# Performance work log

Measured on AMD Instinct MI355X. Metric: run time of the kernel, lower is better.

Reference implementation:

```python
import jax, jax.numpy as jnp
import numpy as np
import math

B, N, DEG, C, F0, NCLS = 128, 512, 8, 128, 128, 10
E = B * N * DEG
RATIO = 0.8
K1 = math.ceil(RATIO * N)    # 410
K2 = math.ceil(RATIO * K1)   # 328
K3 = math.ceil(RATIO * K2)   # 263


def setup_inputs() -> dict:
    key = jax.random.key(0)
    ks = jax.random.split(key, 32)
    x = jax.random.normal(ks[0], (B * N, F0), jnp.float32)
    epg = N * DEG
    src_l = jax.random.randint(ks[1], (B, epg), 0, N)
    dst_l = jax.random.randint(ks[2], (B, epg), 0, N)
    off = (jnp.arange(B, dtype=jnp.int32) * N)[:, None]
    edge_src = (src_l + off).reshape(-1).astype(jnp.int32)
    edge_dst = (dst_l + off).reshape(-1).astype(jnp.int32)

    def lin(k, fi, fo):
        return jax.random.normal(k, (fi, fo), jnp.float32) / np.float32(np.sqrt(fi))

    inp = {"x": x, "edge_src": edge_src, "edge_dst": edge_dst}
    i = 3
    for s, fi in (("1", F0), ("2", C), ("3", C)):
        inp["Wroot" + s] = lin(ks[i], fi, C); i += 1
        inp["Wrel" + s] = lin(ks[i], fi, C); i += 1
        inp["brel" + s] = jnp.zeros((C,), jnp.float32)
        inp["p" + s] = jax.random.normal(ks[i], (C,), jnp.float32); i += 1
    inp["W1"] = lin(ks[i], 2 * C, 128); i += 1
    inp["b1"] = jnp.zeros((128,), jnp.float32)
    inp["W2"] = lin(ks[i], 128, 64); i += 1
    inp["b2"] = jnp.zeros((64,), jnp.float32)
    inp["W3"] = lin(ks[i], 64, NCLS); i += 1
    inp["b3"] = jnp.zeros((NCLS,), jnp.float32)
    return inp


def graph_conv(x, src, dst, emask, Wroot, Wrel, brel, num_nodes):
    # PyG GraphConv (aggr='add'): lin_rel(sum_j x_j) + lin_root(x_i)
    msg = x[src] * emask[:, None]                      # masked gather  [E, C]
    agg = jax.ops.segment_sum(msg, dst, num_segments=num_nodes)
    return agg @ Wrel + brel + x @ Wroot


def topk_pool(x, p, src, dst, emask, b, n, k):
    # score = tanh(x . p / ||p||), keep top-k nodes per graph, scale kept x by score
    score = jnp.tanh((x @ p) / jnp.linalg.norm(p))     # [b*n]
    vals, idx = jax.lax.top_k(score.reshape(b, n), k)  # [b, k]
    perm = (idx + (jnp.arange(b, dtype=idx.dtype) * n)[:, None]).reshape(-1)
    x_new = x[perm] * vals.reshape(-1, 1)
    inv = jnp.full((b * n,), -1, jnp.int32).at[perm].set(
        jnp.arange(b * k, dtype=jnp.int32))
    ns, nd = inv[src], inv[dst]
    nmask = emask * (ns >= 0) * (nd >= 0)
    return x_new, jnp.maximum(ns, 0), jnp.maximum(nd, 0), nmask


def readout(h, b, k):
    hb = h.reshape(b, k, -1)
    return jnp.concatenate([hb.max(axis=1), hb.mean(axis=1)], axis=-1)  # gmp||gap


def reference(x, edge_src, edge_dst,
              Wroot1, Wrel1, brel1, p1,
              Wroot2, Wrel2, brel2, p2,
              Wroot3, Wrel3, brel3, p3,
              W1, b1, W2, b2, W3, b3):
    emask = jnp.ones((E,), x.dtype)
    s, d = edge_src, edge_dst

    h = jax.nn.relu(graph_conv(x, s, d, emask, Wroot1, Wrel1, brel1, B * N))
    h, s, d, emask = topk_pool(h, p1, s, d, emask, B, N, K1)
    x1 = readout(h, B, K1)

    h = jax.nn.relu(graph_conv(h, s, d, emask, Wroot2, Wrel2, brel2, B * K1))
    h, s, d, emask = topk_pool(h, p2, s, d, emask, B, K1, K2)
    x2 = readout(h, B, K2)

    h = jax.nn.relu(graph_conv(h, s, d, emask, Wroot3, Wrel3, brel3, B * K2))
    h, s, d, emask = topk_pool(h, p3, s, d, emask, B, K2, K3)
    x3 = readout(h, B, K3)

    g = x1 + x2 + x3                                   # [B, 256]
    g = jax.nn.relu(g @ W1 + b1)                       # dropout is identity in eval
    g = jax.nn.relu(g @ W2 + b2)
    return jax.nn.log_softmax(g @ W3 + b3, axis=-1)    # [B, NCLS]
```

## Files before the change

kernel.cpp:

```cpp
#include <hip/hip_runtime.h>
#include <hip/hip_bf16.h>
#include <math.h>

#define B_G   128
#define N0    512
#define DEG   8
#define CCH   128
#define EPG   (N0*DEG)
#define E_TOTAL (B_G*EPG)
#define K1    410
#define K2    328
#define K3    263
#define NCLS  10

#define SWZ(row, cb) ((((cb) ^ ((row) & 7)) << 2))

using bf16x8 = __attribute__((ext_vector_type(8))) __bf16;
using f32x4  = __attribute__((ext_vector_type(4))) float;
typedef unsigned short ushort;
typedef unsigned int uint;
typedef unsigned long long u64;

__device__ __forceinline__ ushort f2b(float f) {
    uint u = __float_as_uint(f);
    u += 0x7fffu + ((u >> 16) & 1u);
    return (ushort)(u >> 16);
}
__device__ __forceinline__ float b2f(ushort h) {
    return __uint_as_float(((uint)h) << 16);
}
__device__ __forceinline__ void split2(float v, ushort& hi, ushort& lo) {
    hi = f2b(v);
    lo = f2b(v - b2f(hi));
}
__device__ __forceinline__ uint pksplit(float v) {
    ushort h, l; split2(v, h, l);
    return (uint)h | ((uint)l << 16);
}
__device__ __forceinline__ float unpk(uint u) {
    return __uint_as_float(u << 16) + __uint_as_float(u & 0xffff0000u);
}
__device__ __forceinline__ float keyval(u64 key) {
    uint tu = (uint)(key >> 32);
    uint su = (tu & 0x80000000u) ? (tu & 0x7fffffffu) : ~tu;
    return __uint_as_float(su);
}

__global__ __launch_bounds__(512) void setup_kernel(
        const float* __restrict__ Wrel0, const float* __restrict__ Wroot0,
        const float* __restrict__ Wrel1, const float* __restrict__ Wroot1,
        const float* __restrict__ Wrel2, const float* __restrict__ Wroot2,
        ushort* __restrict__ Bph, ushort* __restrict__ Bpl,
        const int* __restrict__ es, const int* __restrict__ ed,
        int* __restrict__ indptr0, int* __restrict__ counts0, ushort* __restrict__ srclist0) {
    __shared__ uint epk[EPG];
    __shared__ int cnt[512], pref[512], curs[512];
    if (blockIdx.x < B_G) {
        int b = blockIdx.x, tid = threadIdx.x;
        cnt[tid] = 0;
        __syncthreads();
        int base = b * EPG;
        for (int i = tid; i < EPG; i += 512) {
            int s = es[base + i] & (N0 - 1);
            int d = ed[base + i] & (N0 - 1);
            epk[i] = (uint)s | ((uint)d << 16);
            atomicAdd(&cnt[d], 1);
        }
        __syncthreads();
        pref[tid] = cnt[tid];
        __syncthreads();
        for (int off = 1; off < 512; off <<= 1) {
            int v = (tid >= off) ? pref[tid - off] : 0;
            __syncthreads();
            pref[tid] += v;
            __syncthreads();
        }
        int excl = tid ? pref[tid - 1] : 0;
        indptr0[b * N0 + tid] = base + excl;
        counts0[b * N0 + tid] = cnt[tid];
        curs[tid] = excl;
        __syncthreads();
        for (int i = tid; i < EPG; i += 512) {
            uint wv = epk[i];
            int dl = wv >> 16;
            int pos = atomicAdd(&curs[dl], 1);
            srclist0[base + pos] = (ushort)(wv & 0xFFFFu);
        }
    } else {
        int i = (blockIdx.x - B_G) * 512 + threadIdx.x;
        if (i < 3 * 32768) {
            int layer = i >> 15, rem = i & 32767;
            int j = rem & 7, lane = (rem >> 3) & 63, cf = (rem >> 9) & 7, ks = rem >> 12;
            int k = ks * 32 + (lane >> 4) * 8 + j;
            int c = cf * 16 + (lane & 15);
            const float* Wrel  = layer == 0 ? Wrel0  : layer == 1 ? Wrel1  : Wrel2;
            const float* Wroot = layer == 0 ? Wroot0 : layer == 1 ? Wroot1 : Wroot2;
            float v = (k < 128) ? Wrel[k * 128 + c] : Wroot[(k - 128) * 128 + c];
            ushort hi, lo; split2(v, hi, lo);
            Bph[i] = hi; Bpl[i] = lo;
        }
    }
}

__global__ __launch_bounds__(1024) void aggregate0(
        const float* __restrict__ xf,
        const int* __restrict__ indptr, const int* __restrict__ counts,
        const ushort* __restrict__ srclist,
        uint* __restrict__ aggp) {
    extern __shared__ float slab[];
    int b = blockIdx.x >> 2, q = blockIdx.x & 3;
    int tid = threadIdx.x;
    const float4* xf4 = (const float4*)xf;
    for (int t = tid; t < N0 * 8; t += 1024) {
        int nd = t >> 3, c4 = t & 7;
        float4 u = xf4[(size_t)(b * N0 + nd) * 32 + q * 8 + c4];
        *(float4*)&slab[nd * 32 + SWZ(nd, c4)] = u;
    }
    __syncthreads();
    int wave = tid >> 6, lane = tid & 63;
    int gl = lane >> 3, sub = lane & 7;
    for (int g = wave; g < N0 / 8; g += 16) {
        int d = g * 8 + gl;
        int beg = indptr[b * N0 + d];
        int cnt = counts[b * N0 + d];
        float4 acc = make_float4(0.f, 0.f, 0.f, 0.f);
        int id_next = (cnt > 0) ? (int)srclist[beg] : 0;
        for (int j = 0; j < cnt; j++) {
            int id = id_next;
            if (j + 1 < cnt) id_next = (int)srclist[beg + j + 1];
            const float4 v = *(const float4*)&slab[id * 32 + SWZ(id, sub)];
            acc.x += v.x; acc.y += v.y; acc.z += v.z; acc.w += v.w;
        }
        uint4 o;
        o.x = pksplit(acc.x); o.y = pksplit(acc.y);
        o.z = pksplit(acc.z); o.w = pksplit(acc.w);
        *(uint4*)&aggp[(size_t)(b * N0 + d) * CCH + q * 32 + sub * 4] = o;
    }
}

__global__ __launch_bounds__(512, 4) void transform_mfma(
        const uint* __restrict__ aggp, const uint* __restrict__ rootp,
        const float* __restrict__ rootf,
        const ushort* __restrict__ Bph, const ushort* __restrict__ Bpl,
        const float* __restrict__ brel, const float* __restrict__ pvec,
        uint* __restrict__ hout, float* __restrict__ score) {
    __shared__ ushort ldsBh[16384];
    __shared__ ushort ldsBl[16384];
    int tid = threadIdx.x;
    int wave = tid >> 6, lane = tid & 63;
    int r = lane & 15, kb = lane >> 4;
    int rows0 = blockIdx.x * 128 + wave * 16;
    int gid = rows0 + r;

    f32x4 acc[8];
#pragma unroll
    for (int cf = 0; cf < 8; cf++) acc[cf] = (f32x4)(0.f);

    union U16 { uint u[4]; bf16x8 v; };

#pragma unroll
    for (int half = 0; half < 2; half++) {
        if (half) __syncthreads();
#pragma unroll
        for (int i = 0; i < 4; i++) {
            int idx = tid + i * 512;
            ((uint4*)ldsBh)[idx] = ((const uint4*)(Bph + half * 16384))[idx];
            ((uint4*)ldsBl)[idx] = ((const uint4*)(Bpl + half * 16384))[idx];
        }
        __syncthreads();
#pragma unroll
        for (int ks4 = 0; ks4 < 4; ks4++) {
            U16 ah, al;
            if (half && rootf) {
                const float* R = rootf + (size_t)gid * CCH + ks4 * 32 + kb * 8;
                float4 f0 = *(const float4*)R;
                float4 f1 = *(const float4*)(R + 4);
                float c[8] = {f0.x, f0.y, f0.z, f0.w, f1.x, f1.y, f1.z, f1.w};
#pragma unroll
                for (int p2 = 0; p2 < 4; p2++) {
                    ushort h0, l0, h1, l1;
                    split2(c[2 * p2], h0, l0);
                    split2(c[2 * p2 + 1], h1, l1);
                    ah.u[p2] = (uint)h0 | ((uint)h1 << 16);
                    al.u[p2] = (uint)l0 | ((uint)l1 << 16);
                }
            } else {
                const uint* A = half ? rootp : aggp;
                size_t rowbase = (size_t)gid * CCH + ks4 * 32 + kb * 8;
                uint4 ua = *(const uint4*)&A[rowbase];
                uint4 ub = *(const uint4*)&A[rowbase + 4];
                ah.u[0] = (ua.x & 0xffffu) | (ua.y << 16);
                ah.u[1] = (ua.z & 0xffffu) | (ua.w << 16);
                ah.u[2] = (ub.x & 0xffffu) | (ub.y << 16);
                ah.u[3] = (ub.z & 0xffffu) | (ub.w << 16);
                al.u[0] = (ua.x >> 16) | (ua.y & 0xffff0000u);
                al.u[1] = (ua.z >> 16) | (ua.w & 0xffff0000u);
                al.u[2] = (ub.x >> 16) | (ub.y & 0xffff0000u);
                al.u[3] = (ub.z >> 16) | (ub.w & 0xffff0000u);
            }
#pragma unroll
            for (int cf = 0; cf < 8; cf++) {
                bf16x8 bh = *(const bf16x8*)&ldsBh[((ks4 * 8 + cf) * 64 + lane) * 8];
                bf16x8 bl = *(const bf16x8*)&ldsBl[((ks4 * 8 + cf) * 64 + lane) * 8];
                acc[cf] = __builtin_amdgcn_mfma_f32_16x16x32_bf16(ah.v, bl, acc[cf], 0, 0, 0);
                acc[cf] = __builtin_amdgcn_mfma_f32_16x16x32_bf16(al.v, bh, acc[cf], 0, 0, 0);
                acc[cf] = __builtin_amdgcn_mfma_f32_16x16x32_bf16(ah.v, bh, acc[cf], 0, 0, 0);
            }
        }
    }

    float pv[8], bb[8], q = 0.f;
#pragma unroll
    for (int cf = 0; cf < 8; cf++) {
        pv[cf] = pvec[cf * 16 + r];
        bb[cf] = brel[cf * 16 + r];
        q += pv[cf] * pv[cf];
    }
    float dots[4] = {0.f, 0.f, 0.f, 0.f};
#pragma unroll
    for (int cf = 0; cf < 8; cf++) {
#pragma unroll
        for (int reg = 0; reg < 4; reg++) {
            float v = acc[cf][reg] + bb[cf];
            v = v > 0.f ? v : 0.f;
            hout[(size_t)(rows0 + kb * 4 + reg) * CCH + cf * 16 + r] = pksplit(v);
            dots[reg] += v * pv[cf];
        }
    }
#pragma unroll
    for (int off = 1; off < 16; off <<= 1) {
        q += __shfl_xor(q, off);
#pragma unroll
        for (int reg = 0; reg < 4; reg++) dots[reg] += __shfl_xor(dots[reg], off);
    }
    if (r == 0) {
        float inv_norm = rsqrtf(q);
#pragma unroll
        for (int reg = 0; reg < 4; reg++)
            score[rows0 + kb * 4 + reg] = tanhf(dots[reg] * inv_norm);
    }
}

__global__ __launch_bounds__(1024) void pool_kernel(
        const float* __restrict__ score, const uint* __restrict__ hp,
        float* __restrict__ gpart,
        const int* __restrict__ ipt_in, const int* __restrict__ cnt_in,
        const ushort* __restrict__ src_in,
        int* __restrict__ ipt_out, int* __restrict__ cnt_out,
        ushort* __restrict__ src_out,
        uint* __restrict__ pooledX, uint* __restrict__ aggout,
        int n, int k, int do_next) {
    int b = blockIdx.x >> 2, q = blockIdx.x & 3;
    int tid = threadIdx.x;
    __shared__ u64 keys[512];
    __shared__ short invl[512];
    __shared__ float redbuf[1024];
    __shared__ int prefL[512];
    __shared__ int wtot[8], woff[8];
    extern __shared__ float slab[];

    u64 key = 0ull;
    if (tid < 512) {
        if (tid < n) {
            uint u = __float_as_uint(score[b * n + tid]);
            u = (u & 0x80000000u) ? ~u : (u | 0x80000000u);
            key = ((u64)u << 32) | (uint)(~tid);
        }
        invl[tid] = -1;
        for (int kk2 = 2; kk2 <= 64; kk2 <<= 1) {
            for (int j = kk2 >> 1; j > 0; j >>= 1) {
                u64 p = __shfl_xor(key, j);
                bool desc = ((tid & kk2) == 0);
                bool lower = ((tid & j) == 0);
                u64 mx = key > p ? key : p;
                u64 mn = key > p ? p : key;
                key = (desc == lower) ? mx : mn;
            }
        }
    } else {
        for (int t = tid - 512; t < n * 8; t += 512) {
            int nd = t >> 3, c4 = t & 7;
            uint4 u = *(const uint4*)&hp[(size_t)(b * n + nd) * CCH + q * 32 + c4 * 4];
            *(float4*)&slab[nd * 32 + SWZ(nd, c4)] =
                make_float4(unpk(u.x), unpk(u.y), unpk(u.z), unpk(u.w));
        }
    }
    __syncthreads();
    for (int kk2 = 128; kk2 <= 512; kk2 <<= 1) {
        for (int j = kk2 >> 1; j > 0; j >>= 1) {
            if (j >= 64) {
                if (tid < 512) keys[tid] = key;
                __syncthreads();
                if (tid < 512) {
                    u64 p = keys[tid ^ j];
                    bool desc = ((tid & kk2) == 0);
                    bool lower = ((tid & j) == 0);
                    u64 mx = key > p ? key : p;
                    u64 mn = key > p ? p : key;
                    key = (desc == lower) ? mx : mn;
                }
                __syncthreads();
            } else if (tid < 512) {
                u64 p = __shfl_xor(key, j);
                bool desc = ((tid & kk2) == 0);
                bool lower = ((tid & j) == 0);
                u64 mx = key > p ? key : p;
                u64 mn = key > p ? p : key;
                key = (desc == lower) ? mx : mn;
            }
        }
    }
    if (tid < 512) keys[tid] = key;
    __syncthreads();
    if (tid < k) invl[(int)(~(uint)key)] = (short)tid;
    __syncthreads();
    for (int t = tid; t < k * 8; t += 1024) {
        int rank = t >> 3, c4 = t & 7;
        u64 kk = keys[rank];
        int old = (int)(~(uint)kk);
        float v = keyval(kk);
        float* p = &slab[old * 32 + SWZ(old, c4)];
        p[0] *= v; p[1] *= v; p[2] *= v; p[3] *= v;
    }
    __syncthreads();
    if (tid < 512) {
        int w = tid >> 5, ch = tid & 31;
        float mx = -1e30f, sm = 0.f;
        for (int r2 = w; r2 < k; r2 += 16) {
            int old = (int)(~(uint)keys[r2]);
            float v = slab[old * 32 + SWZ(old, ch >> 2) + (ch & 3)];
            mx = fmaxf(mx, v); sm += v;
        }
        redbuf[w * 32 + ch] = mx;
        redbuf[512 + w * 32 + ch] = sm;
    }
    __syncthreads();
    if (tid < 32) {
        float m = -1e30f, s = 0.f;
        for (int w = 0; w < 16; w++) {
            m = fmaxf(m, redbuf[w * 32 + tid]);
            s += redbuf[512 + w * 32 + tid];
        }
        gpart[b * 256 + q * 32 + tid] = m;
        gpart[b * 256 + 128 + q * 32 + tid] = s / (float)k;
    }
    if (!do_next) return;
    for (int t = tid; t < k * 8; t += 1024) {
        int rank = t >> 3, c4 = t & 7;
        int old = (int)(~(uint)keys[rank]);
        const float* p = &slab[old * 32 + SWZ(old, c4)];
        uint4 o;
        o.x = pksplit(p[0]); o.y = pksplit(p[1]);
        o.z = pksplit(p[2]); o.w = pksplit(p[3]);
        *(uint4*)&pooledX[(size_t)(b * k + rank) * CCH + q * 32 + c4 * 4] = o;
    }
    {
        int wave = tid >> 6, lane = tid & 63;
        int gl = lane >> 3, sub = lane & 7;
        int ngroups = (k + 7) >> 3;
        for (int g = wave; g < ngroups; g += 16) {
            int d = g * 8 + gl;
            bool act = d < k;
            int beg = 0, cc = 0;
            if (act) {
                int old = (int)(~(uint)keys[d]);
                beg = ipt_in[b * n + old];
                cc = cnt_in[b * n + old];
            }
            float4 acc = make_float4(0.f, 0.f, 0.f, 0.f);
            int s_next = (cc > 0) ? (int)src_in[beg] : 0;
            for (int j = 0; j < cc; j++) {
                int s = s_next;
                if (j + 1 < cc) s_next = (int)src_in[beg + j + 1];
                if (invl[s] >= 0) {
                    const float4 v = *(const float4*)&slab[s * 32 + SWZ(s, sub)];
                    acc.x += v.x; acc.y += v.y; acc.z += v.z; acc.w += v.w;
                }
            }
            if (act) {
                uint4 o;
                o.x = pksplit(acc.x); o.y = pksplit(acc.y);
                o.z = pksplit(acc.z); o.w = pksplit(acc.w);
                *(uint4*)&aggout[(size_t)(b * k + d) * CCH + q * 32 + sub * 4] = o;
            }
        }
    }
    if (q == 0) {
        int beg = 0, c = 0, nk = 0;
        if (tid < k) {
            int old = (int)(~(uint)keys[tid]);
            beg = ipt_in[b * n + old];
            c = cnt_in[b * n + old];
            for (int t = 0; t < c; t++)
                if (invl[src_in[beg + t]] >= 0) nk++;
        }
        int lane = tid & 63;
        int incl = (tid < 512 && tid < k) ? nk : 0;
#pragma unroll
        for (int o = 1; o < 64; o <<= 1) {
            int t = __shfl_up(incl, o);
            if (lane >= o) incl += t;
        }
        if (tid < 512 && lane == 63) wtot[tid >> 6] = incl;
        __syncthreads();
        if (tid < 8) {
            int s = 0;
            for (int w = 0; w < tid; w++) s += wtot[w];
            woff[tid] = s;
        }
        __syncthreads();
        if (tid < 512) prefL[tid] = incl + woff[tid >> 6];
        __syncthreads();
        if (tid < k) {
            int excl = tid ? prefL[tid - 1] : 0;
            ipt_out[b * k + tid] = b * EPG + excl;
            cnt_out[b * k + tid] = nk;
            int pos = b * EPG + excl;
            for (int t = 0; t < c; t++) {
                int ns = invl[src_in[beg + t]];
                if (ns >= 0) src_out[pos++] = (ushort)ns;
            }
        }
    }
}

__global__ __launch_bounds__(128) void mlp_kernel(const float* __restrict__ gpart,
        const float* __restrict__ W1, const float* __restrict__ b1,
        const float* __restrict__ W2, const float* __restrict__ b2,
        const float* __restrict__ W3, const float* __restrict__ b3,
        float* __restrict__ out) {
    int b = blockIdx.x, t = threadIdx.x;
    __shared__ float gs[256], h1[128], h2[64], lg[10];
    const float* g0 = gpart + ((size_t)0 * B_G + b) * 256;
    const float* g1 = gpart + ((size_t)1 * B_G + b) * 256;
    const float* g2 = gpart + ((size_t)2 * B_G + b) * 256;
    gs[t] = g0[t] + g1[t] + g2[t];
    gs[128 + t] = g0[128 + t] + g1[128 + t] + g2[128 + t];
    __syncthreads();
    {
        float a = b1[t];
        for (int c = 0; c < 256; c++) a += gs[c] * W1[c * 128 + t];
        h1[t] = fmaxf(a, 0.f);
    }
    __syncthreads();
    if (t < 64) {
        float a = b2[t];
        for (int c = 0; c < 128; c++) a += h1[c] * W2[c * 64 + t];
        h2[t] = fmaxf(a, 0.f);
    }
    __syncthreads();
    if (t < 10) {
        float a = b3[t];
        for (int c = 0; c < 64; c++) a += h2[c] * W3[c * 10 + t];
        lg[t] = a;
    }
    __syncthreads();
    if (t < 10) {
        float m = lg[0];
        for (int i = 1; i < 10; i++) m = fmaxf(m, lg[i]);
        float s = 0.f;
        for (int i = 0; i < 10; i++) s += expf(lg[i] - m);
        out[b * 10 + t] = lg[t] - m - logf(s);
    }
}

extern "C" void kernel_launch(void* const* d_in, const int* in_sizes, int n_in,
                              void* d_out, int out_size, void* d_ws, size_t ws_size,
                              hipStream_t stream) {
    (void)in_sizes; (void)n_in; (void)out_size; (void)ws_size;
    const float* x0 = (const float*)d_in[0];
    const int* es = (const int*)d_in[1];
    const int* ed = (const int*)d_in[2];
    const float* Wroot[3] = {(const float*)d_in[3], (const float*)d_in[7], (const float*)d_in[11]};
    const float* Wrel[3]  = {(const float*)d_in[4], (const float*)d_in[8], (const float*)d_in[12]};
    const float* brel[3]  = {(const float*)d_in[5], (const float*)d_in[9], (const float*)d_in[13]};
    const float* pvec[3]  = {(const float*)d_in[6], (const float*)d_in[10], (const float*)d_in[14]};
    const float* W1 = (const float*)d_in[15];
    const float* b1 = (const float*)d_in[16];
    const float* W2 = (const float*)d_in[17];
    const float* b2 = (const float*)d_in[18];
    const float* W3 = (const float*)d_in[19];
    const float* b3 = (const float*)d_in[20];

    size_t off = 0;
    char* base = (char*)d_ws;
    auto alloc = [&](size_t bytes) -> void* {
        void* p = base + off;
        off += (bytes + 255) & ~(size_t)255;
        return p;
    };
    const size_t FEATP = (size_t)(B_G * N0) * CCH * 4;
    uint* P0 = (uint*)alloc(FEATP);
    uint* P1 = (uint*)alloc(FEATP);
    uint* P2 = (uint*)alloc(FEATP);
    ushort* Bph = (ushort*)alloc((size_t)3 * 32768 * 2);
    ushort* Bpl = (ushort*)alloc((size_t)3 * 32768 * 2);
    int* iptA = (int*)alloc((size_t)(B_G * N0) * 4);
    int* cntA = (int*)alloc((size_t)(B_G * N0) * 4);
    ushort* srcA = (ushort*)alloc((size_t)E_TOTAL * 2);
    int* iptB = (int*)alloc((size_t)(B_G * N0) * 4);
    int* cntB = (int*)alloc((size_t)(B_G * N0) * 4);
    ushort* srcB = (ushort*)alloc((size_t)E_TOTAL * 2);
    float* score = (float*)alloc((size_t)(B_G * N0) * 4);
    float* gpart = (float*)alloc((size_t)3 * B_G * 256 * 4);

    setup_kernel<<<B_G + (3 * 32768 + 511) / 512, 512, 0, stream>>>(
        Wrel[0], Wroot[0], Wrel[1], Wroot[1], Wrel[2], Wroot[2],
        Bph, Bpl, es, ed, iptA, cntA, srcA);

    aggregate0<<<4 * B_G, 1024, (size_t)N0 * 32 * 4, stream>>>(
        x0, iptA, cntA, srcA, P1);
    transform_mfma<<<B_G * N0 / 128, 512, 0, stream>>>(
        P1, nullptr, x0, Bph, Bpl, brel[0], pvec[0], P0, score);
    pool_kernel<<<4 * B_G, 1024, (size_t)N0 * 32 * 4, stream>>>(
        score, P0, gpart + (size_t)0 * B_G * 256,
        iptA, cntA, srcA, iptB, cntB, srcB, P2, P1, N0, K1, 1);

    transform_mfma<<<B_G * K1 / 128, 512, 0, stream>>>(
        P1, P2, nullptr, Bph + 32768, Bpl + 32768, brel[1], pvec[1], P0, score);
    pool_kernel<<<4 * B_G, 1024, (size_t)K1 * 32 * 4, stream>>>(
        score, P0, gpart + (size_t)1 * B_G * 256,
        iptB, cntB, srcB, iptA, cntA, srcA, P2, P1, K1, K2, 1);

    transform_mfma<<<B_G * K2 / 128, 512, 0, stream>>>(
        P1, P2, nullptr, Bph + 2 * 32768, Bpl + 2 * 32768, brel[2], pvec[2], P0, score);
    pool_kernel<<<4 * B_G, 1024, (size_t)K2 * 32 * 4, stream>>>(
        score, P0, gpart + (size_t)2 * B_G * 256,
        iptA, cntA, srcA, nullptr, nullptr, nullptr, nullptr, nullptr, K2, K3, 0);

    mlp_kernel<<<B_G, 128, 0, stream>>>(gpart, W1, b1, W2, b2, W3, b3, (float*)d_out);
}
```

Measured before the change: 197.8 us.

## Fuse final top-k pooling and readout into the MLP head kernel

Replaces the last pool_kernel launch (4 blocks per graph, 1024 threads) and the separate MLP kernel with one pool_final kernel per graph. It does a 512-thread bitonic sort of the scores, reads the kept rows directly from global memory to compute the max and mean readout, and then runs the MLP and log-softmax. This removes one launch and the gpart round trip, and skips the slab staging in the final stage, at the cost of fewer, larger blocks (128 instead of 512) doing the final gather. The do_next flag is dropped because the remaining pool_kernel calls always continue.

```diff
diff --git a/kernel.cpp b/kernel.cpp
--- a/kernel.cpp
+++ b/kernel.cpp
@@ -249,7 +249,7 @@
         int* __restrict__ ipt_out, int* __restrict__ cnt_out,
         ushort* __restrict__ src_out,
         uint* __restrict__ pooledX, uint* __restrict__ aggout,
-        int n, int k, int do_next) {
+        int n, int k) {
     int b = blockIdx.x >> 2, q = blockIdx.x & 3;
     int tid = threadIdx.x;
     __shared__ u64 keys[512];
@@ -344,7 +344,6 @@
         gpart[b * 256 + q * 32 + tid] = m;
         gpart[b * 256 + 128 + q * 32 + tid] = s / (float)k;
     }
-    if (!do_next) return;
     for (int t = tid; t < k * 8; t += 1024) {
         int rank = t >> 3, c4 = t & 7;
         int old = (int)(~(uint)keys[rank]);
@@ -424,43 +423,97 @@
     }
 }
 
-__global__ __launch_bounds__(128) void mlp_kernel(const float* __restrict__ gpart,
+__global__ __launch_bounds__(512) void pool_final(
+        const float* __restrict__ score, const uint* __restrict__ hp,
+        const float* __restrict__ gpart,
         const float* __restrict__ W1, const float* __restrict__ b1,
         const float* __restrict__ W2, const float* __restrict__ b2,
         const float* __restrict__ W3, const float* __restrict__ b3,
-        float* __restrict__ out) {
-    int b = blockIdx.x, t = threadIdx.x;
+        float* __restrict__ out, int n, int k) {
+    int b = blockIdx.x, tid = threadIdx.x;
+    __shared__ u64 keys[512];
+    __shared__ float smx[8][128], ssm[8][128];
     __shared__ float gs[256], h1[128], h2[64], lg[10];
-    const float* g0 = gpart + ((size_t)0 * B_G + b) * 256;
-    const float* g1 = gpart + ((size_t)1 * B_G + b) * 256;
-    const float* g2 = gpart + ((size_t)2 * B_G + b) * 256;
-    gs[t] = g0[t] + g1[t] + g2[t];
-    gs[128 + t] = g0[128 + t] + g1[128 + t] + g2[128 + t];
-    __syncthreads();
-    {
-        float a = b1[t];
-        for (int c = 0; c < 256; c++) a += gs[c] * W1[c * 128 + t];
-        h1[t] = fmaxf(a, 0.f);
-    }
-    __syncthreads();
-    if (t < 64) {
-        float a = b2[t];
-        for (int c = 0; c < 128; c++) a += h1[c] * W2[c * 64 + t];
-        h2[t] = fmaxf(a, 0.f);
-    }
-    __syncthreads();
-    if (t < 10) {
-        float a = b3[t];
-        for (int c = 0; c < 64; c++) a += h2[c] * W3[c * 10 + t];
-        lg[t] = a;
-    }
-    __syncthreads();
-    if (t < 10) {
+
+    u64 key = 0ull;
+    if (tid < n) {
+        uint u = __float_as_uint(score[b * n + tid]);
+        u = (u & 0x80000000u) ? ~u : (u | 0x80000000u);
+        key = ((u64)u << 32) | (uint)(~tid);
+    }
+    for (int kk2 = 2; kk2 <= 512; kk2 <<= 1) {
+        for (int j = kk2 >> 1; j > 0; j >>= 1) {
+            if (j >= 64) {
+                keys[tid] = key;
+                __syncthreads();
+                u64 p = keys[tid ^ j];
+                bool desc = ((tid & kk2) == 0);
+                bool lower = ((tid & j) == 0);
+                u64 mx = key > p ? key : p;
+                u64 mn = key > p ? p : key;
+                key = (desc == lower) ? mx : mn;
+                __syncthreads();
+            } else {
+                u64 p = __shfl_xor(key, j);
+                bool desc = ((tid & kk2) == 0);
+                bool lower = ((tid & j) == 0);
+                u64 mx = key > p ? key : p;
+                u64 mn = key > p ? p : key;
+                key = (desc == lower) ? mx : mn;
+            }
+        }
+    }
+    keys[tid] = key;
+    __syncthreads();
+    int wave = tid >> 6, lane = tid & 63;
+    float mx0 = -1e30f, mx1 = -1e30f, sm0 = 0.f, sm1 = 0.f;
+    for (int r = wave; r < k; r += 8) {
+        u64 kk = keys[r];
+        int old = (int)(~(uint)kk);
+        float v = keyval(kk);
+        uint2 u = ((const uint2*)(hp + (size_t)(b * n + old) * CCH))[lane];
+        float c0 = unpk(u.x) * v;
+        float c1 = unpk(u.y) * v;
+        mx0 = fmaxf(mx0, c0); sm0 += c0;
+        mx1 = fmaxf(mx1, c1); sm1 += c1;
+    }
+    smx[wave][2 * lane] = mx0; smx[wave][2 * lane + 1] = mx1;
+    ssm[wave][2 * lane] = sm0; ssm[wave][2 * lane + 1] = sm1;
+    __syncthreads();
+    if (tid < 128) {
+        float m = smx[0][tid], s = ssm[0][tid];
+#pragma unroll
+        for (int w = 1; w < 8; w++) { m = fmaxf(m, smx[w][tid]); s += ssm[w][tid]; }
+        const float* g0 = gpart + ((size_t)0 * B_G + b) * 256;
+        const float* g1 = gpart + ((size_t)1 * B_G + b) * 256;
+        gs[tid] = g0[tid] + g1[tid] + m;
+        gs[128 + tid] = g0[128 + tid] + g1[128 + tid] + s / (float)k;
+    }
+    __syncthreads();
+    if (tid < 128) {
+        float a = b1[tid];
+        for (int c = 0; c < 256; c++) a += gs[c] * W1[c * 128 + tid];
+        h1[tid] = fmaxf(a, 0.f);
+    }
+    __syncthreads();
+    if (tid < 64) {
+        float a = b2[tid];
+        for (int c = 0; c < 128; c++) a += h1[c] * W2[c * 64 + tid];
+        h2[tid] = fmaxf(a, 0.f);
+    }
+    __syncthreads();
+    if (tid < 10) {
+        float a = b3[tid];
+        for (int c = 0; c < 64; c++) a += h2[c] * W3[c * 10 + tid];
+        lg[tid] = a;
+    }
+    __syncthreads();
+    if (tid < 10) {
         float m = lg[0];
         for (int i = 1; i < 10; i++) m = fmaxf(m, lg[i]);
         float s = 0.f;
         for (int i = 0; i < 10; i++) s += expf(lg[i] - m);
-        out[b * 10 + t] = lg[t] - m - logf(s);
+        out[b * 10 + tid] = lg[tid] - m - logf(s);
     }
 }
 
@@ -502,7 +555,7 @@
     int* cntB = (int*)alloc((size_t)(B_G * N0) * 4);
     ushort* srcB = (ushort*)alloc((size_t)E_TOTAL * 2);
     float* score = (float*)alloc((size_t)(B_G * N0) * 4);
-    float* gpart = (float*)alloc((size_t)3 * B_G * 256 * 4);
+    float* gpart = (float*)alloc((size_t)2 * B_G * 256 * 4);
 
     setup_kernel<<<B_G + (3 * 32768 + 511) / 512, 512, 0, stream>>>(
         Wrel[0], Wroot[0], Wrel[1], Wroot[1], Wrel[2], Wroot[2],
@@ -514,19 +567,16 @@
         P1, nullptr, x0, Bph, Bpl, brel[0], pvec[0], P0, score);
     pool_kernel<<<4 * B_G, 1024, (size_t)N0 * 32 * 4, stream>>>(
         score, P0, gpart + (size_t)0 * B_G * 256,
-        iptA, cntA, srcA, iptB, cntB, srcB, P2, P1, N0, K1, 1);
+        iptA, cntA, srcA, iptB, cntB, srcB, P2, P1, N0, K1);
 
     transform_mfma<<<B_G * K1 / 128, 512, 0, stream>>>(
         P1, P2, nullptr, Bph + 32768, Bpl + 32768, brel[1], pvec[1], P0, score);
     pool_kernel<<<4 * B_G, 1024, (size_t)K1 * 32 * 4, stream>>>(
         score, P0, gpart + (size_t)1 * B_G * 256,
-        iptB, cntB, srcB, iptA, cntA, srcA, P2, P1, K1, K2, 1);
+        iptB, cntB, srcB, iptA, cntA, srcA, P2, P1, K1, K2);
 
     transform_mfma<<<B_G * K2 / 128, 512, 0, stream>>>(
         P1, P2, nullptr, Bph + 2 * 32768, Bpl + 2 * 32768, brel[2], pvec[2], P0, score);
-    pool_kernel<<<4 * B_G, 1024, (size_t)K2 * 32 * 4, stream>>>(
-        score, P0, gpart + (size_t)2 * B_G * 256,
-        iptA, cntA, srcA, nullptr, nullptr, nullptr, nullptr, nullptr, K2, K3, 0);
-
-    mlp_kernel<<<B_G, 128, 0, stream>>>(gpart, W1, b1, W2, b2, W3, b3, (float*)d_out);
-}
+    pool_final<<<B_G, 512, 0, stream>>>(
+        score, P0, gpart, W1, b1, W2, b2, W3, b3, (float*)d_out, K2, K3);
+}
```

New measurement: 204.1 us. 1.03x slower.

## Replace bitonic sort in top-k pooling with MSB radix select

Applied to the files above, without the earlier changes.

The full 512-element bitonic sort of 64-bit score keys in pool_kernel is replaced by an 8-bit-digit MSB radix select. It finds the k-th key with shared-memory histograms and a suffix scan, then compacts the selected nodes in original index order through a prefix scan. All 1024 threads now load the feature slab, and scaling and readout walk nodes in index order with a mask. Kept nodes are no longer ordered by score, which is safe because the downstream convolution and readout do not depend on node order. The cost is a variable number of select passes, each with several block barriers, and readout now touches all n nodes instead of k.

```diff
diff --git a/kernel.cpp b/kernel.cpp
--- a/kernel.cpp
+++ b/kernel.cpp
@@ -252,84 +252,110 @@
         int n, int k, int do_next) {
     int b = blockIdx.x >> 2, q = blockIdx.x & 3;
     int tid = threadIdx.x;
-    __shared__ u64 keys[512];
     __shared__ short invl[512];
+    __shared__ short old_of[512];
+    __shared__ float sval[512];
+    __shared__ int hist[256];
+    __shared__ int cum[257];
+    __shared__ int bc[1];
     __shared__ float redbuf[1024];
     __shared__ int prefL[512];
     __shared__ int wtot[8], woff[8];
     extern __shared__ float slab[];
 
     u64 key = 0ull;
-    if (tid < 512) {
-        if (tid < n) {
-            uint u = __float_as_uint(score[b * n + tid]);
-            u = (u & 0x80000000u) ? ~u : (u | 0x80000000u);
-            key = ((u64)u << 32) | (uint)(~tid);
-        }
-        invl[tid] = -1;
-        for (int kk2 = 2; kk2 <= 64; kk2 <<= 1) {
-            for (int j = kk2 >> 1; j > 0; j >>= 1) {
-                u64 p = __shfl_xor(key, j);
-                bool desc = ((tid & kk2) == 0);
-                bool lower = ((tid & j) == 0);
-                u64 mx = key > p ? key : p;
-                u64 mn = key > p ? p : key;
-                key = (desc == lower) ? mx : mn;
-            }
-        }
-    } else {
-        for (int t = tid - 512; t < n * 8; t += 512) {
-            int nd = t >> 3, c4 = t & 7;
-            uint4 u = *(const uint4*)&hp[(size_t)(b * n + nd) * CCH + q * 32 + c4 * 4];
-            *(float4*)&slab[nd * 32 + SWZ(nd, c4)] =
-                make_float4(unpk(u.x), unpk(u.y), unpk(u.z), unpk(u.w));
-        }
-    }
-    __syncthreads();
-    for (int kk2 = 128; kk2 <= 512; kk2 <<= 1) {
-        for (int j = kk2 >> 1; j > 0; j >>= 1) {
-            if (j >= 64) {
-                if (tid < 512) keys[tid] = key;
-                __syncthreads();
-                if (tid < 512) {
-                    u64 p = keys[tid ^ j];
-                    bool desc = ((tid & kk2) == 0);
-                    bool lower = ((tid & j) == 0);
-                    u64 mx = key > p ? key : p;
-                    u64 mn = key > p ? p : key;
-                    key = (desc == lower) ? mx : mn;
-                }
-                __syncthreads();
-            } else if (tid < 512) {
-                u64 p = __shfl_xor(key, j);
-                bool desc = ((tid & kk2) == 0);
-                bool lower = ((tid & j) == 0);
-                u64 mx = key > p ? key : p;
-                u64 mn = key > p ? p : key;
-                key = (desc == lower) ? mx : mn;
-            }
-        }
-    }
-    if (tid < 512) keys[tid] = key;
-    __syncthreads();
-    if (tid < k) invl[(int)(~(uint)key)] = (short)tid;
-    __syncthreads();
-    for (int t = tid; t < k * 8; t += 1024) {
-        int rank = t >> 3, c4 = t & 7;
-        u64 kk = keys[rank];
-        int old = (int)(~(uint)kk);
-        float v = keyval(kk);
-        float* p = &slab[old * 32 + SWZ(old, c4)];
-        p[0] *= v; p[1] *= v; p[2] *= v; p[3] *= v;
+    bool has = (tid < n);
+    if (has) {
+        uint u = __float_as_uint(score[b * n + tid]);
+        u = (u & 0x80000000u) ? ~u : (u | 0x80000000u);
+        key = ((u64)u << 32) | (uint)(~tid);
+        sval[tid] = keyval(key);
+    }
+    for (int t = tid; t < n * 8; t += 1024) {
+        int nd = t >> 3, c4 = t & 7;
+        uint4 u = *(const uint4*)&hp[(size_t)(b * n + nd) * CCH + q * 32 + c4 * 4];
+        *(float4*)&slab[nd * 32 + SWZ(nd, c4)] =
+            make_float4(unpk(u.x), unpk(u.y), unpk(u.z), unpk(u.w));
+    }
+    bool active = has, sure = false;
+    int rem = k;
+    for (int pass = 0; pass < 8; pass++) {
+        int dig = (int)((key >> (56 - 8 * pass)) & 255);
+        if (tid < 256) hist[tid] = 0;
+        __syncthreads();
+        if (active) atomicAdd(&hist[dig], 1);
+        __syncthreads();
+        if (tid < 64) {
+            int b0 = hist[tid * 4], b1 = hist[tid * 4 + 1];
+            int b2 = hist[tid * 4 + 2], b3 = hist[tid * 4 + 3];
+            int s = b0 + b1 + b2 + b3;
+            int suf = s;
+#pragma unroll
+            for (int o = 1; o < 64; o <<= 1) {
+                int t2 = __shfl_down(suf, o);
+                if (tid + o < 64) suf += t2;
+            }
+            int after = suf - s;
+            cum[tid * 4 + 3] = after + b3;
+            cum[tid * 4 + 2] = after + b3 + b2;
+            cum[tid * 4 + 1] = after + b3 + b2 + b1;
+            cum[tid * 4 + 0] = after + s;
+            if (tid == 0) cum[256] = 0;
+        }
+        __syncthreads();
+        if (tid < 256 && cum[tid] >= rem && cum[tid + 1] < rem) bc[0] = tid;
+        __syncthreads();
+        int dstar = bc[0];
+        int hcnt = hist[dstar];
+        rem -= cum[dstar + 1];
+        if (active) {
+            if (dig > dstar) { sure = true; active = false; }
+            else if (dig < dstar) active = false;
+        }
+        __syncthreads();
+        if (hcnt == 1) break;
+    }
+    bool sel = sure || (active && rem > 0);
+    {
+        int lane = tid & 63;
+        int v = sel ? 1 : 0;
+        int incl = v;
+#pragma unroll
+        for (int o = 1; o < 64; o <<= 1) {
+            int t2 = __shfl_up(incl, o);
+            if (lane >= o) incl += t2;
+        }
+        if (tid < 512 && lane == 63) wtot[tid >> 6] = incl;
+        __syncthreads();
+        if (tid < 8) {
+            int s = 0;
+            for (int w = 0; w < tid; w++) s += wtot[w];
+            woff[tid] = s;
+        }
+        __syncthreads();
+        if (tid < 512) {
+            int rank = incl - v + woff[tid >> 6];
+            invl[tid] = sel ? (short)rank : (short)-1;
+            if (sel) old_of[rank] = (short)tid;
+        }
+        __syncthreads();
+    }
+    for (int t = tid; t < n * 8; t += 1024) {
+        int nd = t >> 3, c4 = t & 7;
+        if (invl[nd] >= 0) {
+            float v = sval[nd];
+            float* p = &slab[nd * 32 + SWZ(nd, c4)];
+            p[0] *= v; p[1] *= v; p[2] *= v; p[3] *= v;
+        }
     }
     __syncthreads();
     if (tid < 512) {
         int w = tid >> 5, ch = tid & 31;
+        int cb = ch >> 2, ce = ch & 3;
         float mx = -1e30f, sm = 0.f;
-        for (int r2 = w; r2 < k; r2 += 16) {
-            int old = (int)(~(uint)keys[r2]);
-            float v = slab[old * 32 + SWZ(old, ch >> 2) + (ch & 3)];
-            mx = fmaxf(mx, v); sm += v;
+        for (int nd = w; nd < n; nd += 16) {
+            float v = slab[nd * 32 + SWZ(nd, cb) + ce];
+            if (invl[nd] >= 0) { mx = fmaxf(mx, v); sm += v; }
         }
         redbuf[w * 32 + ch] = mx;
         redbuf[512 + w * 32 + ch] = sm;
@@ -347,7 +373,7 @@
     if (!do_next) return;
     for (int t = tid; t < k * 8; t += 1024) {
         int rank = t >> 3, c4 = t & 7;
-        int old = (int)(~(uint)keys[rank]);
+        int old = (int)old_of[rank];
         const float* p = &slab[old * 32 + SWZ(old, c4)];
         uint4 o;
         o.x = pksplit(p[0]); o.y = pksplit(p[1]);
@@ -363,7 +389,7 @@
             bool act = d < k;
             int beg = 0, cc = 0;
             if (act) {
-                int old = (int)(~(uint)keys[d]);
+                int old = (int)old_of[d];
                 beg = ipt_in[b * n + old];
                 cc = cnt_in[b * n + old];
             }
@@ -388,7 +414,7 @@
     if (q == 0) {
         int beg = 0, c = 0, nk = 0;
         if (tid < k) {
-            int old = (int)(~(uint)keys[tid]);
+            int old = (int)old_of[tid];
             beg = ipt_in[b * n + old];
             c = cnt_in[b * n + old];
             for (int t = 0; t < c; t++)
@@ -398,8 +424,8 @@
         int incl = (tid < 512 && tid < k) ? nk : 0;
 #pragma unroll
         for (int o = 1; o < 64; o <<= 1) {
-            int t = __shfl_up(incl, o);
-            if (lane >= o) incl += t;
+            int t2 = __shfl_up(incl, o);
+            if (lane >= o) incl += t2;
         }
         if (tid < 512 && lane == 63) wtot[tid >> 6] = incl;
         __syncthreads();
```

New measurement: 199.6 us. No clear change (+0.9%).
